# Performance work log

Measured on AMD Instinct MI355X. Metric: run time of the kernel, lower is better.

Reference implementation:

```python
import jax, jax.numpy as jnp
import numpy as np

DIM = 1024
NHEAD = 16
HEAD_DIM = DIM // NHEAD


def setup_inputs() -> dict:
    key = jax.random.key(0)
    k_x, k_wqkv, k_bqkv, k_wp, k_bp = jax.random.split(key, 5)
    scale = 1.0 / np.sqrt(DIM)
    return {
        "x": jax.random.normal(k_x, (4, 2048, DIM), dtype=jnp.float32),
        "w_qkv": jax.random.uniform(k_wqkv, (DIM, 3 * DIM), minval=-scale, maxval=scale, dtype=jnp.float32),
        "b_qkv": jax.random.uniform(k_bqkv, (3 * DIM,), minval=-scale, maxval=scale, dtype=jnp.float32),
        "w_proj": jax.random.uniform(k_wp, (DIM, DIM), minval=-scale, maxval=scale, dtype=jnp.float32),
        "b_proj": jax.random.uniform(k_bp, (DIM,), minval=-scale, maxval=scale, dtype=jnp.float32),
    }


def reference(x, w_qkv, b_qkv, w_proj, b_proj):
    B, N, D = x.shape
    # qkv projection: [B,N,3D] -> [3,B,H,N,hd]
    qkv = x @ w_qkv + b_qkv
    qkv = qkv.reshape(B, N, 3, NHEAD, HEAD_DIM).transpose(2, 0, 3, 1, 4)
    q, k, v = qkv[0], qkv[1], qkv[2]
    # naive full attention: scores [B,H,N,N]
    attn = jnp.einsum("bhqd,bhkd->bhqk", q, k) / jnp.sqrt(jnp.float32(HEAD_DIM))
    attn = jax.nn.softmax(attn, axis=-1)
    out = jnp.einsum("bhqk,bhkd->bhqd", attn, v)  # [B,H,N,hd]
    out = out.transpose(0, 2, 1, 3).reshape(B, N, D)
    return out @ w_proj + b_proj
```

## Files before the change

kernel.cpp:

```cpp
#include <hip/hip_runtime.h>
#include <math.h>

#define DIM     1024
#define NHEAD   16
#define HD      64
#define BATCH   4
#define SEQ     2048
#define MTOT    (BATCH * SEQ)
#define QKV_N   (3 * DIM)

typedef __attribute__((ext_vector_type(8))) short bf16x8;
typedef __attribute__((ext_vector_type(4))) float f32x4;
typedef unsigned int u32;
typedef unsigned short u16;

__device__ __forceinline__ u16 f2bf(float f) {
    u32 u = __float_as_uint(f);
    return (u16)((u + 0x7fffu + ((u >> 16) & 1u)) >> 16);
}

__device__ __forceinline__ float exp2_fast(float x) {
    float r; asm("v_exp_f32 %0, %1" : "=v"(r) : "v"(x)); return r;
}

__device__ __forceinline__ u32 cvtpk_bf16(float lo, float hi) {
    u32 r; asm("v_cvt_pk_bf16_f32 %0, %1, %2" : "=v"(r) : "v"(lo), "v"(hi));
    return r;
}

__device__ __forceinline__ void gload_lds16(const u16* g, u16* l) {
    __builtin_amdgcn_global_load_lds((const __attribute__((address_space(1))) u32*)g,
                                     (__attribute__((address_space(3))) u32*)l, 16, 0, 0);
}

__global__ __launch_bounds__(256) void prep(
    const float* __restrict__ x,  u16* __restrict__ xb,
    const float* __restrict__ wq, u16* __restrict__ wqt,
    const float* __restrict__ wp, u16* __restrict__ wpt)
{
    const int b = blockIdx.x;
    if (b < 8192) {
        const int i = (b * 256 + threadIdx.x) * 4;
        const float4 v = *(const float4*)&x[i];
        ushort4 o;
        o.x = f2bf(v.x); o.y = f2bf(v.y); o.z = f2bf(v.z); o.w = f2bf(v.w);
        *(ushort4*)&xb[i] = o;
        return;
    }
    __shared__ float Ls[64][65];
    int i = b - 8192;
    const float* W; u16* Wt; int N;
    if (i < 768) { W = wq; Wt = wqt; N = QKV_N; }
    else         { i -= 768; W = wp; Wt = wpt; N = DIM; }
    const int k0 = (i & 15) * 64, n0 = (i >> 4) * 64;
    const int t = threadIdx.x;
    const int r = t >> 4, c4 = (t & 15) << 2;
    #pragma unroll
    for (int j = 0; j < 4; ++j) {
        const float4 v = *(const float4*)&W[(size_t)(k0 + r + j * 16) * N + n0 + c4];
        Ls[r + j * 16][c4 + 0] = v.x; Ls[r + j * 16][c4 + 1] = v.y;
        Ls[r + j * 16][c4 + 2] = v.z; Ls[r + j * 16][c4 + 3] = v.w;
    }
    __syncthreads();
    #pragma unroll
    for (int j = 0; j < 4; ++j) {
        const int nr = r + j * 16;
        ushort4 o;
        o.x = f2bf(Ls[c4 + 0][nr]); o.y = f2bf(Ls[c4 + 1][nr]);
        o.z = f2bf(Ls[c4 + 2][nr]); o.w = f2bf(Ls[c4 + 3][nr]);
        *(ushort4*)&Wt[(size_t)(n0 + nr) * DIM + k0 + c4] = o;
    }
}

#define GEMM_STAGE(buf, kof, Aptr, Bptr)                                       \
    _Pragma("unroll") for (int i = 0; i < 2; ++i) {                            \
        const int row = w * 32 + i * 16 + (lane >> 2);                         \
        const int slot = (lane & 3) ^ ((row >> 1) & 3);                        \
        gload_lds16(&Aptr[(size_t)(m0 + row) * DIM + (kof) + slot * 8],        \
                    &As[buf][(w * 32 + i * 16) * 32]);                         \
        gload_lds16(&Bptr[(size_t)(n0 + row) * DIM + (kof) + slot * 8],        \
                    &Bs[buf][(w * 32 + i * 16) * 32]);                         \
    }

#define GEMM_MAINLOOP(Aptr, Bptr)                                              \
    __shared__ __align__(16) u16 As[2][128 * 32];                              \
    __shared__ __align__(16) u16 Bs[2][128 * 32];                              \
    const int t = threadIdx.x;                                                 \
    const int lane = t & 63, w = t >> 6;                                       \
    const int n0 = blockIdx.x * 128;                                           \
    const int m0 = blockIdx.y * 128;                                           \
    const int wm = (w & 1) * 64, wn = (w >> 1) * 64;                           \
    const int g = lane >> 4, li = lane & 15;                                   \
    f32x4 acc[4][4];                                                           \
    _Pragma("unroll") for (int mt = 0; mt < 4; ++mt)                           \
        _Pragma("unroll") for (int nt = 0; nt < 4; ++nt)                       \
            acc[mt][nt] = (f32x4){0.f, 0.f, 0.f, 0.f};                         \
    GEMM_STAGE(0, 0, Aptr, Bptr)                                               \
    __syncthreads();                                                           \
    int cur = 0;                                                               \
    for (int k0 = 0; k0 < DIM; k0 += 32) {                                     \
        if (k0 + 32 < DIM) { GEMM_STAGE(cur ^ 1, k0 + 32, Aptr, Bptr) }        \
        bf16x8 a[4], b[4];                                                     \
        _Pragma("unroll") for (int mt = 0; mt < 4; ++mt) {                     \
            const int row = wm + mt * 16 + li;                                 \
            const int slot = g ^ ((row >> 1) & 3);                             \
            a[mt] = *(const bf16x8*)&As[cur][row * 32 + slot * 8];             \
        }                                                                      \
        _Pragma("unroll") for (int nt = 0; nt < 4; ++nt) {                     \
            const int row = wn + nt * 16 + li;                                 \
            const int slot = g ^ ((row >> 1) & 3);                             \
            b[nt] = *(const bf16x8*)&Bs[cur][row * 32 + slot * 8];             \
        }                                                                      \
        _Pragma("unroll") for (int mt = 0; mt < 4; ++mt)                       \
            _Pragma("unroll") for (int nt = 0; nt < 4; ++nt)                   \
                acc[mt][nt] = __builtin_amdgcn_mfma_f32_16x16x32_bf16(         \
                    a[mt], b[nt], acc[mt][nt], 0, 0, 0);                       \
        __syncthreads();                                                       \
        cur ^= 1;                                                              \
    }

#define QSCALE 0.18033688011112042f
__global__ __launch_bounds__(256) void gemm_qkv(
    const u16* __restrict__ A, const u16* __restrict__ Bt,
    const float* __restrict__ bias,
    u16* __restrict__ qo, u16* __restrict__ ko, u16* __restrict__ vo)
{
    GEMM_MAINLOOP(A, Bt)
    #pragma unroll
    for (int nt = 0; nt < 4; ++nt) {
        const int n = n0 + wn + nt * 16 + li;
        const int which = n >> 10;
        const int head  = (n >> 6) & 15;
        const int hd    = n & 63;
        const float bv = bias[n];
        if (which == 2) {
            #pragma unroll
            for (int mt = 0; mt < 4; ++mt) {
                const int m = m0 + wm + mt * 16 + g * 4;
                const int bb = m >> 11, tok = m & 2047;
                const u32 p0 = cvtpk_bf16(acc[mt][nt][0] + bv, acc[mt][nt][1] + bv);
                const u32 p1 = cvtpk_bf16(acc[mt][nt][2] + bv, acc[mt][nt][3] + bv);
                u16* d = &vo[((size_t)(bb * NHEAD + head) * HD + hd) * SEQ + tok];
                *(u32*)&d[0] = p0;
                *(u32*)&d[2] = p1;
            }
        } else {
            u16* dst = (which == 0) ? qo : ko;
            const float scale = (which == 0) ? QSCALE : 1.0f;
            #pragma unroll
            for (int mt = 0; mt < 4; ++mt) {
                #pragma unroll
                for (int r = 0; r < 4; ++r) {
                    const int m = m0 + wm + mt * 16 + g * 4 + r;
                    const int bb = m >> 11, tok = m & 2047;
                    dst[((size_t)(bb * NHEAD + head) * SEQ + tok) * HD + hd] =
                        f2bf((acc[mt][nt][r] + bv) * scale);
                }
            }
        }
    }
}

__global__ __launch_bounds__(256) void gemm_proj(
    const u16* __restrict__ A, const u16* __restrict__ Bt,
    const float* __restrict__ bias, float* __restrict__ out)
{
    GEMM_MAINLOOP(A, Bt)
    #pragma unroll
    for (int nt = 0; nt < 4; ++nt) {
        const int n = n0 + wn + nt * 16 + li;
        const float bv = bias[n];
        #pragma unroll
        for (int mt = 0; mt < 4; ++mt) {
            #pragma unroll
            for (int r = 0; r < 4; ++r) {
                const int m = m0 + wm + mt * 16 + g * 4 + r;
                out[(size_t)m * DIM + n] = acc[mt][nt][r] + bv;
            }
        }
    }
}

#define NKT  (SEQ / 64)
#define ATTN_STAGE(buf, ktile)                                                 \
    {                                                                          \
        gload_lds16(&kg[(size_t)(ktile) * (64 * HD) + (size_t)key * HD + sl],  \
                    &Ks[buf][(w * 8) * 64]);                                   \
        gload_lds16(&vg[(size_t)rho * SEQ + (ktile) * 64 + sl],                \
                    &Vs[buf][(w * 8) * 64]);                                   \
    }

__global__ __launch_bounds__(512) void attn_mfma(
    const u16* __restrict__ q, const u16* __restrict__ k,
    const u16* __restrict__ v, u16* __restrict__ ao)
{
    __shared__ __align__(16) u16 Ks[2][64 * 64];
    __shared__ __align__(16) u16 Vs[2][64 * 64];

    const int t = threadIdx.x;
    const int lane = t & 63, w = t >> 6;
    const int g = lane >> 4, li = lane & 15;

    int flat = blockIdx.y * 8 + blockIdx.x;
    flat = (flat & 7) * 64 + (flat >> 3);
    const int q0 = (flat & 7) * 256;
    const int bh = flat >> 3;
    const size_t base = (size_t)bh * SEQ * HD;
    const u16* kg = k + base;
    const u16* vg = v + (size_t)bh * HD * SEQ;

    bf16x8 qf[2][2];
    #pragma unroll
    for (int h = 0; h < 2; ++h) {
        const size_t qrow = base + (size_t)(q0 + w * 32 + h * 16 + li) * HD;
        qf[h][0] = *(const bf16x8*)&q[qrow + g * 8];
        qf[h][1] = *(const bf16x8*)&q[qrow + 32 + g * 8];
    }

    float lsum[2] = {0.f, 0.f};
    f32x4 oacc[2][4];
    #pragma unroll
    for (int h = 0; h < 2; ++h)
        #pragma unroll
        for (int nt = 0; nt < 4; ++nt) oacc[h][nt] = (f32x4){0.f, 0.f, 0.f, 0.f};

    const int srow = lane >> 3;
    const int sslot = lane & 7;
    const int rho = w * 8 + srow;
    const int key = (rho & 32) | (((rho >> 2) & 3) << 3)
                  | (((rho >> 4) & 1) << 2) | (rho & 3);
    const int sl = (sslot ^ (rho & 7)) << 3;
    const int x8 = li & 7;

    ATTN_STAGE(0, 0)
    __syncthreads();

    int cur = 0;
    for (int kt = 0; kt < NKT; ++kt) {
        if (kt + 1 < NKT) { ATTN_STAGE(cur ^ 1, kt + 1) }
        const u16* Kc = Ks[cur];
        const u16* Vc = Vs[cur];

        f32x4 s[2][4];
        __builtin_amdgcn_s_setprio(1);
        #pragma unroll
        for (int nt = 0; nt < 4; ++nt) {
            const int rowb = (nt * 16 + li) << 6;
            const bf16x8 kf0 = *(const bf16x8*)&Kc[rowb + ((g ^ x8) << 3)];
            const bf16x8 kf1 = *(const bf16x8*)&Kc[rowb + (((g ^ 4) ^ x8) << 3)];
            #pragma unroll
            for (int h = 0; h < 2; ++h) {
                f32x4 c = (f32x4){0.f, 0.f, 0.f, 0.f};
                c = __builtin_amdgcn_mfma_f32_16x16x32_bf16(kf0, qf[h][0], c, 0, 0, 0);
                c = __builtin_amdgcn_mfma_f32_16x16x32_bf16(kf1, qf[h][1], c, 0, 0, 0);
                s[h][nt] = c;
            }
        }
        __builtin_amdgcn_s_setprio(0);

        bf16x8 pb[2][2];
        #pragma unroll
        for (int h = 0; h < 2; ++h) {
            float rs = 0.f;
            #pragma unroll
            for (int nt = 0; nt < 4; ++nt)
                #pragma unroll
                for (int r = 0; r < 4; ++r) {
                    const float p = exp2_fast(s[h][nt][r]);
                    s[h][nt][r] = p;
                    rs += p;
                }
            lsum[h] += rs;
            #pragma unroll
            for (int ks = 0; ks < 2; ++ks) {
                union { u32 u[4]; bf16x8 v8; } uu;
                uu.u[0] = cvtpk_bf16(s[h][2 * ks][0],     s[h][2 * ks][1]);
                uu.u[1] = cvtpk_bf16(s[h][2 * ks][2],     s[h][2 * ks][3]);
                uu.u[2] = cvtpk_bf16(s[h][2 * ks + 1][0], s[h][2 * ks + 1][1]);
                uu.u[3] = cvtpk_bf16(s[h][2 * ks + 1][2], s[h][2 * ks + 1][3]);
                pb[h][ks] = uu.v8;
            }
        }

        __builtin_amdgcn_s_setprio(1);
        #pragma unroll
        for (int ks = 0; ks < 2; ++ks) {
            #pragma unroll
            for (int nt = 0; nt < 4; ++nt) {
                const bf16x8 vb = *(const bf16x8*)
                    &Vc[((nt * 16 + li) << 6) + (((g ^ (ks << 2)) ^ x8) << 3)];
                #pragma unroll
                for (int h = 0; h < 2; ++h)
                    oacc[h][nt] = __builtin_amdgcn_mfma_f32_16x16x32_bf16(
                        vb, pb[h][ks], oacc[h][nt], 0, 0, 0);
            }
        }
        __builtin_amdgcn_s_setprio(0);

        __syncthreads();
        cur ^= 1;
    }

    const int bb = bh >> 4, hh = bh & 15;
    #pragma unroll
    for (int h = 0; h < 2; ++h) {
        float lf = lsum[h];
        lf += __shfl_xor(lf, 16);
        lf += __shfl_xor(lf, 32);
        const float inv = 1.0f / lf;
        const int tok = q0 + w * 32 + h * 16 + li;
        u16* dst = &ao[(size_t)(bb * SEQ + tok) * DIM + hh * HD];
        #pragma unroll
        for (int nt = 0; nt < 4; ++nt) {
            const u32 p0 = cvtpk_bf16(oacc[h][nt][0] * inv, oacc[h][nt][1] * inv);
            const u32 p1 = cvtpk_bf16(oacc[h][nt][2] * inv, oacc[h][nt][3] * inv);
            *(u32*)&dst[nt * 16 + g * 4]     = p0;
            *(u32*)&dst[nt * 16 + g * 4 + 2] = p1;
        }
    }
}

extern "C" void kernel_launch(void* const* d_in, const int* in_sizes, int n_in,
                              void* d_out, int out_size, void* d_ws, size_t ws_size,
                              hipStream_t stream)
{
    const float* x      = (const float*)d_in[0];
    const float* w_qkv  = (const float*)d_in[1];
    const float* b_qkv  = (const float*)d_in[2];
    const float* w_proj = (const float*)d_in[3];
    const float* b_proj = (const float*)d_in[4];
    float* out = (float*)d_out;

    u16* xb  = (u16*)d_ws;
    u16* wqt = xb  + (size_t)MTOT * DIM;
    u16* wpt = wqt + (size_t)QKV_N * DIM;
    u16* qb  = wpt + (size_t)DIM * DIM;
    u16* kb  = qb  + (size_t)MTOT * DIM;
    u16* vb  = kb  + (size_t)MTOT * DIM;
    u16* aob = vb  + (size_t)MTOT * DIM;

    prep<<<8192 + 768 + 256, 256, 0, stream>>>(x, xb, w_qkv, wqt, w_proj, wpt);
    gemm_qkv<<<dim3(QKV_N / 128, MTOT / 128), 256, 0, stream>>>(xb, wqt, b_qkv, qb, kb, vb);
    attn_mfma<<<dim3(SEQ / 256, BATCH * NHEAD), 512, 0, stream>>>(qb, kb, vb, aob);
    gemm_proj<<<dim3(DIM / 128, MTOT / 128), 256, 0, stream>>>(aob, wpt, b_proj, out);
}
```

Baseline: 189.4 us.

## Software-pipeline attention loop: overlap PV of previous tile with QK of current

Restructures the attention key loop into a skewed software pipeline. Each iteration computes QK for tile kt, then PV for tile kt-1 using probabilities from the previous iteration, then the softmax exponentials for tile kt. LDS buffers grow from double to triple buffering to keep the previous V tile resident. The aim is to give the scheduler independent MFMA and exp work to interleave, hiding softmax latency behind matrix ops, at the cost of more LDS and registers and a more complex prologue and epilogue.

After: 196.5 us. 3.8% more time.

```diff
diff --git a/kernel.cpp b/kernel.cpp
--- a/kernel.cpp
+++ b/kernel.cpp
@@ -182,6 +182,7 @@
 }
 
 #define NKT  (SEQ / 64)
+#define ROT3(c) ((c) == 2 ? 0 : (c) + 1)
 #define ATTN_STAGE(buf, ktile)                                                 \
     {                                                                          \
         gload_lds16(&kg[(size_t)(ktile) * (64 * HD) + (size_t)key * HD + sl],  \
@@ -190,12 +191,75 @@
                     &Vs[buf][(w * 8) * 64]);                                   \
     }
 
+#define ATTN_QK(KCP)                                                           \
+    __builtin_amdgcn_s_setprio(1);                                             \
+    _Pragma("unroll") for (int nt = 0; nt < 4; ++nt) {                         \
+        const int rowb = (nt * 16 + li) << 6;                                  \
+        const bf16x8 kf0 = *(const bf16x8*)&KCP[rowb + ((g ^ x8) << 3)];       \
+        const bf16x8 kf1 = *(const bf16x8*)&KCP[rowb + (((g ^ 4) ^ x8) << 3)]; \
+        _Pragma("unroll") for (int h = 0; h < 2; ++h) {                        \
+            f32x4 c = (f32x4){0.f, 0.f, 0.f, 0.f};                             \
+            c = __builtin_amdgcn_mfma_f32_16x16x32_bf16(kf0, qf[h][0], c, 0, 0, 0); \
+            c = __builtin_amdgcn_mfma_f32_16x16x32_bf16(kf1, qf[h][1], c, 0, 0, 0); \
+            s[h][nt] = c;                                                      \
+        }                                                                      \
+    }                                                                          \
+    __builtin_amdgcn_s_setprio(0);
+
+#define ATTN_PV(VCP, PB)                                                       \
+    __builtin_amdgcn_s_setprio(1);                                             \
+    _Pragma("unroll") for (int ks = 0; ks < 2; ++ks) {                         \
+        _Pragma("unroll") for (int nt = 0; nt < 4; ++nt) {                     \
+            const bf16x8 vb = *(const bf16x8*)                                 \
+                &VCP[((nt * 16 + li) << 6) + (((g ^ (ks << 2)) ^ x8) << 3)];   \
+            _Pragma("unroll") for (int h = 0; h < 2; ++h)                      \
+                oacc[h][nt] = __builtin_amdgcn_mfma_f32_16x16x32_bf16(         \
+                    vb, PB[h][ks], oacc[h][nt], 0, 0, 0);                      \
+        }                                                                      \
+    }                                                                          \
+    __builtin_amdgcn_s_setprio(0);
+
+#define ATTN_SM(PB)                                                            \
+    _Pragma("unroll") for (int h = 0; h < 2; ++h) {                            \
+        float rs = 0.f;                                                        \
+        _Pragma("unroll") for (int nt = 0; nt < 4; ++nt)                       \
+            _Pragma("unroll") for (int r = 0; r < 4; ++r) {                    \
+                const float p = exp2_fast(s[h][nt][r]);                        \
+                s[h][nt][r] = p;                                               \
+                rs += p;                                                       \
+            }                                                                  \
+        lsum[h] += rs;                                                         \
+        _Pragma("unroll") for (int ks = 0; ks < 2; ++ks) {                     \
+            union { u32 u[4]; bf16x8 v8; } uu;                                 \
+            uu.u[0] = cvtpk_bf16(s[h][2 * ks][0],     s[h][2 * ks][1]);        \
+            uu.u[1] = cvtpk_bf16(s[h][2 * ks][2],     s[h][2 * ks][3]);        \
+            uu.u[2] = cvtpk_bf16(s[h][2 * ks + 1][0], s[h][2 * ks + 1][1]);    \
+            uu.u[3] = cvtpk_bf16(s[h][2 * ks + 1][2], s[h][2 * ks + 1][3]);    \
+            PB[h][ks] = uu.v8;                                                 \
+        }                                                                      \
+    }
+
+#define ATTN_ITER(PBPREV, PBCUR, DOSTAGE)                                      \
+    {                                                                          \
+        const int ns  = ROT3(cs);                                              \
+        const int vsl = ROT3(ns);                                \
+        if (DOSTAGE) { ATTN_STAGE(ns, kt + 1) }                                \
+        const u16* Kc = Ks[cs];                                                \
+        const u16* Vc = Vs[vsl];                                               \
+        f32x4 s[2][4];                                                         \
+        ATTN_QK(Kc)                                                            \
+        ATTN_PV(Vc, PBPREV)                                                    \
+        ATTN_SM(PBCUR)                                                         \
+        __syncthreads();                                                       \
+        cs = ns; ++kt;                                                         \
+    }
+
 __global__ __launch_bounds__(512) void attn_mfma(
     const u16* __restrict__ q, const u16* __restrict__ k,
     const u16* __restrict__ v, u16* __restrict__ ao)
 {
-    __shared__ __align__(16) u16 Ks[2][64 * 64];
-    __shared__ __align__(16) u16 Vs[2][64 * 64];
+    __shared__ __align__(16) u16 Ks[3][64 * 64];
+    __shared__ __align__(16) u16 Vs[3][64 * 64];
 
     const int t = threadIdx.x;
     const int lane = t & 63, w = t >> 6;
@@ -232,73 +296,30 @@
     const int sl = (sslot ^ (rho & 7)) << 3;
     const int x8 = li & 7;
 
+    bf16x8 pbA[2][2], pbB[2][2];
+
     ATTN_STAGE(0, 0)
     __syncthreads();
-
-    int cur = 0;
-    for (int kt = 0; kt < NKT; ++kt) {
-        if (kt + 1 < NKT) { ATTN_STAGE(cur ^ 1, kt + 1) }
-        const u16* Kc = Ks[cur];
-        const u16* Vc = Vs[cur];
-
+    ATTN_STAGE(1, 1)
+    {
+        const u16* Kc = Ks[0];
         f32x4 s[2][4];
-        __builtin_amdgcn_s_setprio(1);
-        #pragma unroll
-        for (int nt = 0; nt < 4; ++nt) {
-            const int rowb = (nt * 16 + li) << 6;
-            const bf16x8 kf0 = *(const bf16x8*)&Kc[rowb + ((g ^ x8) << 3)];
-            const bf16x8 kf1 = *(const bf16x8*)&Kc[rowb + (((g ^ 4) ^ x8) << 3)];
-            #pragma unroll
-            for (int h = 0; h < 2; ++h) {
-                f32x4 c = (f32x4){0.f, 0.f, 0.f, 0.f};
-                c = __builtin_amdgcn_mfma_f32_16x16x32_bf16(kf0, qf[h][0], c, 0, 0, 0);
-                c = __builtin_amdgcn_mfma_f32_16x16x32_bf16(kf1, qf[h][1], c, 0, 0, 0);
-                s[h][nt] = c;
-            }
-        }
-        __builtin_amdgcn_s_setprio(0);
-
-        bf16x8 pb[2][2];
-        #pragma unroll
-        for (int h = 0; h < 2; ++h) {
-            float rs = 0.f;
-            #pragma unroll
-            for (int nt = 0; nt < 4; ++nt)
-                #pragma unroll
-                for (int r = 0; r < 4; ++r) {
-                    const float p = exp2_fast(s[h][nt][r]);
-                    s[h][nt][r] = p;
-                    rs += p;
-                }
-            lsum[h] += rs;
-            #pragma unroll
-            for (int ks = 0; ks < 2; ++ks) {
-                union { u32 u[4]; bf16x8 v8; } uu;
-                uu.u[0] = cvtpk_bf16(s[h][2 * ks][0],     s[h][2 * ks][1]);
-                uu.u[1] = cvtpk_bf16(s[h][2 * ks][2],     s[h][2 * ks][3]);
-                uu.u[2] = cvtpk_bf16(s[h][2 * ks + 1][0], s[h][2 * ks + 1][1]);
-                uu.u[3] = cvtpk_bf16(s[h][2 * ks + 1][2], s[h][2 * ks + 1][3]);
-                pb[h][ks] = uu.v8;
-            }
-        }
-
-        __builtin_amdgcn_s_setprio(1);
-        #pragma unroll
-        for (int ks = 0; ks < 2; ++ks) {
-            #pragma unroll
-            for (int nt = 0; nt < 4; ++nt) {
-                const bf16x8 vb = *(const bf16x8*)
-                    &Vc[((nt * 16 + li) << 6) + (((g ^ (ks << 2)) ^ x8) << 3)];
-                #pragma unroll
-                for (int h = 0; h < 2; ++h)
-                    oacc[h][nt] = __builtin_amdgcn_mfma_f32_16x16x32_bf16(
-                        vb, pb[h][ks], oacc[h][nt], 0, 0, 0);
-            }
-        }
-        __builtin_amdgcn_s_setprio(0);
-
-        __syncthreads();
-        cur ^= 1;
+        ATTN_QK(Kc)
+        ATTN_SM(pbA)
+    }
+    __syncthreads();
+
+    int kt = 1, cs = 1;
+    while (kt + 1 < NKT) {
+        ATTN_ITER(pbA, pbB, 1)
+        ATTN_ITER(pbB, pbA, 1)
+    }
+    ATTN_ITER(pbA, pbB, 0)
+
+    {
+        const int vsl = ROT3(ROT3(cs));
+        const u16* Vc = Vs[vsl];
+        ATTN_PV(Vc, pbB)
     }
 
     const int bb = bh >> 4, hh = bh & 15;
```

## Split attention key range across two blocks and merge partials in separate kernel

Applied to the files above, without the earlier changes.

The attention kernel now splits the key sequence into two halves, so twice as many blocks run, each over half the keys. Each block writes unnormalized fp16 partial outputs and row sums to workspace. A new merge kernel adds the two partials, normalizes them and writes the bf16 attention output. The aim is more parallelism and shorter per-block loops. In exchange it adds an extra launch and tens of MB of partial-result traffic, and it risks fp16 range and precision loss on the unnormalized accumulators.

Result: slower. 198.1 us (+4.6%).

```diff
diff --git a/kernel.cpp b/kernel.cpp
--- a/kernel.cpp
+++ b/kernel.cpp
@@ -25,6 +25,11 @@
 
 __device__ __forceinline__ u32 cvtpk_bf16(float lo, float hi) {
     u32 r; asm("v_cvt_pk_bf16_f32 %0, %1, %2" : "=v"(r) : "v"(lo), "v"(hi));
+    return r;
+}
+
+__device__ __forceinline__ u32 cvtpk_f16(float lo, float hi) {
+    u32 r; asm("v_cvt_pkrtz_f16_f32 %0, %1, %2" : "=v"(r) : "v"(lo), "v"(hi));
     return r;
 }
 
@@ -192,7 +197,7 @@
 
 __global__ __launch_bounds__(512) void attn_mfma(
     const u16* __restrict__ q, const u16* __restrict__ k,
-    const u16* __restrict__ v, u16* __restrict__ ao)
+    const u16* __restrict__ v, u16* __restrict__ po, float* __restrict__ pl)
 {
     __shared__ __align__(16) u16 Ks[2][64 * 64];
     __shared__ __align__(16) u16 Vs[2][64 * 64];
@@ -201,10 +206,11 @@
     const int lane = t & 63, w = t >> 6;
     const int g = lane >> 4, li = lane & 15;
 
-    int flat = blockIdx.y * 8 + blockIdx.x;
-    flat = (flat & 7) * 64 + (flat >> 3);
-    const int q0 = (flat & 7) * 256;
-    const int bh = flat >> 3;
+    int flat = blockIdx.y * 16 + blockIdx.x;
+    flat = (flat & 7) * 128 + (flat >> 3);
+    const int bh   = flat >> 4;
+    const int half = (flat >> 3) & 1;
+    const int q0   = (flat & 7) * 256;
     const size_t base = (size_t)bh * SEQ * HD;
     const u16* kg = k + base;
     const u16* vg = v + (size_t)bh * HD * SEQ;
@@ -232,12 +238,13 @@
     const int sl = (sslot ^ (rho & 7)) << 3;
     const int x8 = li & 7;
 
-    ATTN_STAGE(0, 0)
+    const int kt0 = half * (NKT / 2);
+    ATTN_STAGE(0, kt0)
     __syncthreads();
 
     int cur = 0;
-    for (int kt = 0; kt < NKT; ++kt) {
-        if (kt + 1 < NKT) { ATTN_STAGE(cur ^ 1, kt + 1) }
+    for (int kt = kt0; kt < kt0 + NKT / 2; ++kt) {
+        if (kt + 1 < kt0 + NKT / 2) { ATTN_STAGE(cur ^ 1, kt + 1) }
         const u16* Kc = Ks[cur];
         const u16* Vc = Vs[cur];
 
@@ -301,23 +308,44 @@
         cur ^= 1;
     }
 
-    const int bb = bh >> 4, hh = bh & 15;
+    u16*  poW = po + ((size_t)(half * 64 + bh) * 2048) * 64;
+    float* plW = pl + (size_t)(half * 64 + bh) * 2048;
     #pragma unroll
     for (int h = 0; h < 2; ++h) {
         float lf = lsum[h];
         lf += __shfl_xor(lf, 16);
         lf += __shfl_xor(lf, 32);
-        const float inv = 1.0f / lf;
         const int tok = q0 + w * 32 + h * 16 + li;
-        u16* dst = &ao[(size_t)(bb * SEQ + tok) * DIM + hh * HD];
+        if (g == 0) plW[tok] = lf;
         #pragma unroll
         for (int nt = 0; nt < 4; ++nt) {
-            const u32 p0 = cvtpk_bf16(oacc[h][nt][0] * inv, oacc[h][nt][1] * inv);
-            const u32 p1 = cvtpk_bf16(oacc[h][nt][2] * inv, oacc[h][nt][3] * inv);
-            *(u32*)&dst[nt * 16 + g * 4]     = p0;
-            *(u32*)&dst[nt * 16 + g * 4 + 2] = p1;
-        }
-    }
+            const u32 p0 = cvtpk_f16(oacc[h][nt][0], oacc[h][nt][1]);
+            const u32 p1 = cvtpk_f16(oacc[h][nt][2], oacc[h][nt][3]);
+            *(u32*)&poW[(size_t)tok * 64 + nt * 16 + g * 4]     = p0;
+            *(u32*)&poW[(size_t)tok * 64 + nt * 16 + g * 4 + 2] = p1;
+        }
+    }
+}
+
+__global__ __launch_bounds__(256) void attn_merge(
+    const u16* __restrict__ po, const float* __restrict__ pl,
+    u16* __restrict__ ao)
+{
+    const size_t e = ((size_t)blockIdx.x * 256 + threadIdx.x) * 8;
+    const int hd8 = (int)(e & 63);
+    const int tok = (int)((e >> 6) & 2047);
+    const int bh  = (int)(e >> 17);
+    union { uint4 u; _Float16 h[8]; } a, b;
+    a.u = *(const uint4*)&po[((size_t)bh * 2048 + tok) * 64 + hd8];
+    b.u = *(const uint4*)&po[((size_t)(64 + bh) * 2048 + tok) * 64 + hd8];
+    const float inv = 1.0f / (pl[bh * 2048 + tok] + pl[(64 + bh) * 2048 + tok]);
+    const int bb = bh >> 4, hh = bh & 15;
+    u32 o[4];
+    #pragma unroll
+    for (int i = 0; i < 4; ++i)
+        o[i] = cvtpk_bf16(((float)a.h[2 * i]     + (float)b.h[2 * i])     * inv,
+                          ((float)a.h[2 * i + 1] + (float)b.h[2 * i + 1]) * inv);
+    *(uint4*)&ao[((size_t)(bb * SEQ + tok)) * DIM + hh * HD + hd8] = *(uint4*)o;
 }
 
 extern "C" void kernel_launch(void* const* d_in, const int* in_sizes, int n_in,
@@ -338,9 +366,12 @@
     u16* kb  = qb  + (size_t)MTOT * DIM;
     u16* vb  = kb  + (size_t)MTOT * DIM;
     u16* aob = vb  + (size_t)MTOT * DIM;
+    u16* po  = aob + (size_t)MTOT * DIM;
+    float* pl = (float*)(po + (size_t)2 * 64 * 2048 * 64);
 
     prep<<<8192 + 768 + 256, 256, 0, stream>>>(x, xb, w_qkv, wqt, w_proj, wpt);
     gemm_qkv<<<dim3(QKV_N / 128, MTOT / 128), 256, 0, stream>>>(xb, wqt, b_qkv, qb, kb, vb);
-    attn_mfma<<<dim3(SEQ / 256, BATCH * NHEAD), 512, 0, stream>>>(qb, kb, vb, aob);
+    attn_mfma<<<dim3(16, BATCH * NHEAD), 512, 0, stream>>>(qb, kb, vb, po, pl);
+    attn_merge<<<(64 * 2048 * 64) / (256 * 8), 256, 0, stream>>>(po, pl, aob);
     gemm_proj<<<dim3(DIM / 128, MTOT / 128), 256, 0, stream>>>(aob, wpt, b_proj, out);
 }
```
